# Kernel optimization log

Hardware: AMD Instinct MI355X
Metric: run time of the kernel (lower is better)

Reference implementation:

```python
import jax, jax.numpy as jnp
import numpy as np

B, T, I, H, O = 256, 512, 128, 512, 64
ALPHA = 0.2          # cfg.leak
BETA = 8.0           # cfg.softplus_beta
THRESH = 20.0        # cfg.softplus_threshold


def _phi(x):
    # F.softplus(x, beta, threshold): linear when beta*x > threshold
    z = BETA * x
    return jnp.where(z > THRESH, x, jax.nn.softplus(jnp.minimum(z, THRESH)) / BETA)


def setup_inputs() -> dict:
    key = jax.random.key(0)
    ks = jax.random.split(key, 6)
    x = jax.random.normal(ks[0], (B, T, I), dtype=jnp.float32)
    W_xh = jax.random.normal(ks[1], (H, I), dtype=jnp.float32) * (1.0 / np.sqrt(I))
    # E/I structure: column-wise sign (abs weights * sign), scaled to modest spectral radius
    sign = np.ones(H, dtype=np.float32)
    perm = np.random.default_rng(0).permutation(H)
    sign[perm[int(round(0.8 * H)):]] = -1.0
    W_hh = jnp.abs(jax.random.normal(ks[2], (H, H), dtype=jnp.float32)) * jnp.asarray(sign)[None, :]
    W_hh = W_hh * (1.2 / (jnp.linalg.norm(W_hh, ord=2) + 1e-6))
    b_h = jnp.zeros((H,), dtype=jnp.float32)
    W_out = jax.random.normal(ks[3], (O, H), dtype=jnp.float32) * (1.0 / np.sqrt(H))
    b_out = jnp.zeros((O,), dtype=jnp.float32)
    return {"x": x, "W_xh": W_xh, "W_hh": W_hh, "b_h": b_h, "W_out": W_out, "b_out": b_out}


def reference(x, W_xh, W_hh, b_h, W_out, b_out):
    # precompute input projection: [B,T,H]
    xw = jnp.einsum('bti,hi->bth', x, W_xh)

    def step(h, xw_t):  # h: [B,H], xw_t: [B,H]
        pre = xw_t + h @ W_hh.T + b_h
        h = (1.0 - ALPHA) * h + ALPHA * _phi(pre)
        y = h @ W_out.T + b_out  # readout='all'
        return h, y

    h0 = jnp.zeros((x.shape[0], W_hh.shape[0]), dtype=x.dtype)
    _, ys = jax.lax.scan(step, h0, jnp.swapaxes(xw, 0, 1))  # ys: [T,B,O]
    return jnp.swapaxes(ys, 0, 1)  # [B,T,O]
```

## Files before the change

### kernel.cpp

```cpp
#include <hip/hip_runtime.h>


#define BB 256
#define TT 512
#define II 128
#define HH 512
#define OO 64
#define RG 16
#define JC 64
#define NG 16
#define NC 8

typedef _Float16 f16;
typedef f16 f16x8 __attribute__((ext_vector_type(8)));
typedef float f32x4 __attribute__((ext_vector_type(4)));

__global__ __launch_bounds__(256, 1)
void eirnn_persist(const float* __restrict__ x,
                   const float* __restrict__ Wxh,
                   const float* __restrict__ Whh,
                   const float* __restrict__ bh,
                   const float* __restrict__ Wout,
                   const float* __restrict__ bout,
                   float* __restrict__ yout,
                   unsigned long long* __restrict__ hbuf)
{
    const int tid  = threadIdx.x;
    const int bid  = blockIdx.x;
    const int wave = tid >> 6;
    const int lane = tid & 63;
    const int quad = lane >> 4;
    const int l16  = lane & 15;
    const int r    = bid >> 3;
    const int c    = bid & 7;
    const int rowbase = r * RG;
    const int jbase   = c * JC;
    const int myrow   = wave * 16 + l16;

    __shared__ __align__(16) f16 hg[2][RG][HH + 8];
    __shared__ __align__(16) f16 xsh[2][RG][II + 8];

    f16x8 bf[16];
    f16x8 xbf[4];
    f16x8 bfo[2];
    {
        const float* wp = Whh + (size_t)(jbase + myrow) * HH + quad * 8;
        #pragma unroll
        for (int ks = 0; ks < 16; ++ks) {
            float4 u = *(const float4*)(wp + ks * 32);
            float4 v = *(const float4*)(wp + ks * 32 + 4);
            f16x8 tv;
            tv[0]=(f16)u.x; tv[1]=(f16)u.y; tv[2]=(f16)u.z; tv[3]=(f16)u.w;
            tv[4]=(f16)v.x; tv[5]=(f16)v.y; tv[6]=(f16)v.z; tv[7]=(f16)v.w;
            bf[ks] = tv;
        }
        const float* wq = Wxh + (size_t)(jbase + myrow) * II + quad * 8;
        #pragma unroll
        for (int ks = 0; ks < 4; ++ks) {
            float4 u = *(const float4*)(wq + ks * 32);
            float4 v = *(const float4*)(wq + ks * 32 + 4);
            f16x8 tv;
            tv[0]=(f16)u.x; tv[1]=(f16)u.y; tv[2]=(f16)u.z; tv[3]=(f16)u.w;
            tv[4]=(f16)v.x; tv[5]=(f16)v.y; tv[6]=(f16)v.z; tv[7]=(f16)v.w;
            xbf[ks] = tv;
        }
        const float* wo = Wout + (size_t)myrow * HH + c * 64 + quad * 8;
        #pragma unroll
        for (int ks = 0; ks < 2; ++ks) {
            float4 u = *(const float4*)(wo + ks * 32);
            float4 v = *(const float4*)(wo + ks * 32 + 4);
            f16x8 tv;
            tv[0]=(f16)u.x; tv[1]=(f16)u.y; tv[2]=(f16)u.z; tv[3]=(f16)u.w;
            tv[4]=(f16)v.x; tv[5]=(f16)v.y; tv[6]=(f16)v.z; tv[7]=(f16)v.w;
            bfo[ks] = tv;
        }
    }
    const float biash = bh[jbase + myrow];
    const float biaso = (c == 0) ? bout[myrow] : 0.0f;

    for (int p = tid; p < RG * (HH + 8); p += 256)
        ((unsigned int*)hg)[p] = 0u;

    float hreg[4] = {0.f, 0.f, 0.f, 0.f};

    const int j8     = tid;
    const int gshard = j8 >> 5;

    float4 xpf0, xpf1;
    {
        int p0 = tid, p1 = tid + 256;
        xpf0 = ((const float4*)(x + ((size_t)(rowbase + (p0 >> 5)) * TT + 0) * II))[p0 & 31];
        xpf1 = ((const float4*)(x + ((size_t)(rowbase + (p1 >> 5)) * TT + 0) * II))[p1 & 31];
    }

    __syncthreads();

    for (int t = 0; t <= TT; ++t) {
        const int pcur = t & 1;

        if (t < TT) {
            int p0 = tid, p1 = tid + 256;
            f16* d0 = &xsh[pcur][p0 >> 5][(p0 & 31) * 4];
            d0[0]=(f16)xpf0.x; d0[1]=(f16)xpf0.y; d0[2]=(f16)xpf0.z; d0[3]=(f16)xpf0.w;
            f16* d1 = &xsh[pcur][p1 >> 5][(p1 & 31) * 4];
            d1[0]=(f16)xpf1.x; d1[1]=(f16)xpf1.y; d1[2]=(f16)xpf1.z; d1[3]=(f16)xpf1.w;
        }
        if (t + 1 < TT) {
            int p0 = tid, p1 = tid + 256;
            xpf0 = ((const float4*)(x + ((size_t)(rowbase + (p0 >> 5)) * TT + (t + 1)) * II))[p0 & 31];
            xpf1 = ((const float4*)(x + ((size_t)(rowbase + (p1 >> 5)) * TT + (t + 1)) * II))[p1 & 31];
        }
        if (t >= 1 && gshard != c) {
            const unsigned long long* src = hbuf
                + (size_t)pcur * (BB * HH / 2)
                + (size_t)rowbase * (HH / 2) + j8;
            const unsigned int tg = (unsigned)t;
            unsigned long long v[16];
            #pragma unroll
            for (int i = 0; i < 16; ++i)
                v[i] = __hip_atomic_load(src + (size_t)i * (HH / 2),
                                         __ATOMIC_RELAXED, __HIP_MEMORY_SCOPE_AGENT);
            for (;;) {
                bool any = false;
                #pragma unroll
                for (int i = 0; i < 16; ++i)
                    any |= ((unsigned)(v[i] >> 32) != tg);
                if (!any) break;
                #pragma unroll
                for (int i = 0; i < 16; ++i)
                    if ((unsigned)(v[i] >> 32) != tg)
                        v[i] = __hip_atomic_load(src + (size_t)i * (HH / 2),
                                                 __ATOMIC_RELAXED, __HIP_MEMORY_SCOPE_AGENT);
            }
            #pragma unroll
            for (int i = 0; i < 16; ++i)
                *(unsigned int*)&hg[pcur][i][j8 * 2] = (unsigned int)v[i];
        }
        __syncthreads();

        if (t < TT) {
            f32x4 acc0 = {0.f,0.f,0.f,0.f}, acc1 = {0.f,0.f,0.f,0.f};
            #pragma unroll
            for (int ks = 0; ks < 16; ks += 2) {
                f16x8 a0 = *(const f16x8*)&hg[pcur][l16][ks * 32 + quad * 8];
                f16x8 a1 = *(const f16x8*)&hg[pcur][l16][(ks + 1) * 32 + quad * 8];
                acc0 = __builtin_amdgcn_mfma_f32_16x16x32_f16(a0, bf[ks], acc0, 0, 0, 0);
                acc1 = __builtin_amdgcn_mfma_f32_16x16x32_f16(a1, bf[ks + 1], acc1, 0, 0, 0);
            }
            #pragma unroll
            for (int ks = 0; ks < 4; ks += 2) {
                f16x8 a0 = *(const f16x8*)&xsh[pcur][l16][ks * 32 + quad * 8];
                f16x8 a1 = *(const f16x8*)&xsh[pcur][l16][(ks + 1) * 32 + quad * 8];
                acc0 = __builtin_amdgcn_mfma_f32_16x16x32_f16(a0, xbf[ks], acc0, 0, 0, 0);
                acc1 = __builtin_amdgcn_mfma_f32_16x16x32_f16(a1, xbf[ks + 1], acc1, 0, 0, 0);
            }
            unsigned long long* dst64 = hbuf + (size_t)((t + 1) & 1) * (BB * HH / 2);
            const unsigned long long tagw = ((unsigned long long)(unsigned)(t + 1)) << 32;
            unsigned int hb[4];
            #pragma unroll
            for (int reg = 0; reg < 4; ++reg) {
                float pre = acc0[reg] + acc1[reg] + biash;
                float z = 8.f * pre;
                float ph = (z > 20.f) ? pre : (__logf(1.f + __expf(z)) * 0.125f);
                float hn = 0.8f * hreg[reg] + 0.2f * ph;
                hreg[reg] = hn;
                hb[reg] = (unsigned int)__builtin_bit_cast(unsigned short, (f16)hn);
            }
            #pragma unroll
            for (int reg = 0; reg < 4; ++reg) {
                unsigned int ob = (unsigned int)__shfl_xor((int)hb[reg], 1, 64);
                if ((lane & 1) == 0) {
                    unsigned int pair = hb[reg] | (ob << 16);
                    size_t eidx = (size_t)(rowbase + quad * 4 + reg) * HH + jbase + myrow;
                    __hip_atomic_store(dst64 + (eidx >> 1), tagw | (unsigned long long)pair,
                                       __ATOMIC_RELAXED, __HIP_MEMORY_SCOPE_AGENT);
                    *(unsigned int*)&hg[(t + 1) & 1][quad * 4 + reg][jbase + myrow] = pair;
                }
            }
        }

        if (t >= 1) {
            f32x4 ya = {0.f,0.f,0.f,0.f};
            f16x8 a0 = *(const f16x8*)&hg[pcur][l16][c * 64 + quad * 8];
            f16x8 a1 = *(const f16x8*)&hg[pcur][l16][c * 64 + 32 + quad * 8];
            ya = __builtin_amdgcn_mfma_f32_16x16x32_f16(a0, bfo[0], ya, 0, 0, 0);
            ya = __builtin_amdgcn_mfma_f32_16x16x32_f16(a1, bfo[1], ya, 0, 0, 0);
            #pragma unroll
            for (int reg = 0; reg < 4; ++reg)
                atomicAdd(yout + ((size_t)(rowbase + quad * 4 + reg) * TT + (t - 1)) * OO + myrow,
                          ya[reg] + biaso);
        }
    }
}

extern "C" void kernel_launch(void* const* d_in, const int* in_sizes, int n_in,
                              void* d_out, int out_size, void* d_ws, size_t ws_size,
                              hipStream_t stream)
{
    const float* x    = (const float*)d_in[0];
    const float* Wxh  = (const float*)d_in[1];
    const float* Whh  = (const float*)d_in[2];
    const float* bh   = (const float*)d_in[3];
    const float* Wout = (const float*)d_in[4];
    const float* bout = (const float*)d_in[5];
    float* yout = (float*)d_out;

    unsigned long long* hbuf = (unsigned long long*)d_ws;
    const size_t hbuf_bytes = (size_t)2 * BB * (HH / 2) * sizeof(unsigned long long);

    if (ws_size < hbuf_bytes) return;

    hipMemsetAsync(hbuf, 0, hbuf_bytes, stream);
    hipMemsetAsync(yout, 0, (size_t)out_size * sizeof(float), stream);

    eirnn_persist<<<dim3(NG * NC), dim3(256), 0, stream>>>(
        x, Wxh, Whh, bh, Wout, bout, yout, hbuf);
}
```

Before: 1.396 ms.

## Split hidden dimension across two 1024-thread blocks per row group instead of eight

```diff
diff --git a/kernel.cpp b/kernel.cpp
--- a/kernel.cpp
+++ b/kernel.cpp
@@ -7,15 +7,15 @@
 #define HH 512
 #define OO 64
 #define RG 16
-#define JC 64
+#define JC 256
 #define NG 16
-#define NC 8
+#define NC 2
 
 typedef _Float16 f16;
 typedef f16 f16x8 __attribute__((ext_vector_type(8)));
 typedef float f32x4 __attribute__((ext_vector_type(4)));
 
-__global__ __launch_bounds__(256, 1)
+__global__ __launch_bounds__(1024, 1)
 void eirnn_persist(const float* __restrict__ x,
                    const float* __restrict__ Wxh,
                    const float* __restrict__ Whh,
@@ -31,8 +31,8 @@
     const int lane = tid & 63;
     const int quad = lane >> 4;
     const int l16  = lane & 15;
-    const int r    = bid >> 3;
-    const int c    = bid & 7;
+    const int r    = bid >> 1;
+    const int c    = bid & 1;
     const int rowbase = r * RG;
     const int jbase   = c * JC;
     const int myrow   = wave * 16 + l16;
@@ -43,6 +43,8 @@
     f16x8 bf[16];
     f16x8 xbf[4];
     f16x8 bfo[2];
+    const int koff = c * 256 + (wave >> 2) * 64;
+    const int ocol = (wave & 3) * 16 + l16;
     {
         const float* wp = Whh + (size_t)(jbase + myrow) * HH + quad * 8;
         #pragma unroll
@@ -64,7 +66,7 @@
             tv[4]=(f16)v.x; tv[5]=(f16)v.y; tv[6]=(f16)v.z; tv[7]=(f16)v.w;
             xbf[ks] = tv;
         }
-        const float* wo = Wout + (size_t)myrow * HH + c * 64 + quad * 8;
+        const float* wo = Wout + (size_t)ocol * HH + koff + quad * 8;
         #pragma unroll
         for (int ks = 0; ks < 2; ++ks) {
             float4 u = *(const float4*)(wo + ks * 32);
@@ -76,120 +78,122 @@
         }
     }
     const float biash = bh[jbase + myrow];
-    const float biaso = (c == 0) ? bout[myrow] : 0.0f;
-
-    for (int p = tid; p < RG * (HH + 8); p += 256)
-        ((unsigned int*)hg)[p] = 0u;
+    const float biaso = (c == 0 && (wave >> 2) == 0) ? bout[ocol] : 0.0f;
+
+    for (int p4 = tid; p4 < RG * (HH + 8) / 2; p4 += 1024)
+        ((unsigned int*)hg)[p4] = 0u;
+
+    float4 xpf;
+    if (tid < 512) {
+        float4 v = ((const float4*)(x + ((size_t)(rowbase + (tid >> 5)) * TT + 0) * II))[tid & 31];
+        f16* d = &xsh[0][tid >> 5][(tid & 31) * 4];
+        d[0]=(f16)v.x; d[1]=(f16)v.y; d[2]=(f16)v.z; d[3]=(f16)v.w;
+        xpf = ((const float4*)(x + ((size_t)(rowbase + (tid >> 5)) * TT + 1) * II))[tid & 31];
+    }
 
     float hreg[4] = {0.f, 0.f, 0.f, 0.f};
 
-    const int j8     = tid;
-    const int gshard = j8 >> 5;
-
-    float4 xpf0, xpf1;
-    {
-        int p0 = tid, p1 = tid + 256;
-        xpf0 = ((const float4*)(x + ((size_t)(rowbase + (p0 >> 5)) * TT + 0) * II))[p0 & 31];
-        xpf1 = ((const float4*)(x + ((size_t)(rowbase + (p1 >> 5)) * TT + 0) * II))[p1 & 31];
-    }
-
-    __syncthreads();
-
-    for (int t = 0; t <= TT; ++t) {
-        const int pcur = t & 1;
-
-        if (t < TT) {
-            int p0 = tid, p1 = tid + 256;
-            f16* d0 = &xsh[pcur][p0 >> 5][(p0 & 31) * 4];
-            d0[0]=(f16)xpf0.x; d0[1]=(f16)xpf0.y; d0[2]=(f16)xpf0.z; d0[3]=(f16)xpf0.w;
-            f16* d1 = &xsh[pcur][p1 >> 5][(p1 & 31) * 4];
-            d1[0]=(f16)xpf1.x; d1[1]=(f16)xpf1.y; d1[2]=(f16)xpf1.z; d1[3]=(f16)xpf1.w;
-        }
-        if (t + 1 < TT) {
-            int p0 = tid, p1 = tid + 256;
-            xpf0 = ((const float4*)(x + ((size_t)(rowbase + (p0 >> 5)) * TT + (t + 1)) * II))[p0 & 31];
-            xpf1 = ((const float4*)(x + ((size_t)(rowbase + (p1 >> 5)) * TT + (t + 1)) * II))[p1 & 31];
-        }
-        if (t >= 1 && gshard != c) {
-            const unsigned long long* src = hbuf
-                + (size_t)pcur * (BB * HH / 2)
-                + (size_t)rowbase * (HH / 2) + j8;
-            const unsigned int tg = (unsigned)t;
-            unsigned long long v[16];
-            #pragma unroll
-            for (int i = 0; i < 16; ++i)
-                v[i] = __hip_atomic_load(src + (size_t)i * (HH / 2),
-                                         __ATOMIC_RELAXED, __HIP_MEMORY_SCOPE_AGENT);
-            for (;;) {
-                bool any = false;
-                #pragma unroll
-                for (int i = 0; i < 16; ++i)
-                    any |= ((unsigned)(v[i] >> 32) != tg);
-                if (!any) break;
-                #pragma unroll
-                for (int i = 0; i < 16; ++i)
-                    if ((unsigned)(v[i] >> 32) != tg)
-                        v[i] = __hip_atomic_load(src + (size_t)i * (HH / 2),
-                                                 __ATOMIC_RELAXED, __HIP_MEMORY_SCOPE_AGENT);
+    const int prow = tid >> 7;
+    const int pj   = (1 - c) * 128 + (tid & 127);
+
+    for (int t = 0; t < TT; ++t) {
+        const int p  = t & 1;
+        const int pn = p ^ 1;
+        __syncthreads();
+
+        f32x4 acc0 = {0.f,0.f,0.f,0.f}, acc1 = {0.f,0.f,0.f,0.f};
+        #pragma unroll
+        for (int ks = 0; ks < 16; ks += 2) {
+            f16x8 a0 = *(const f16x8*)&hg[p][l16][ks * 32 + quad * 8];
+            f16x8 a1 = *(const f16x8*)&hg[p][l16][(ks + 1) * 32 + quad * 8];
+            acc0 = __builtin_amdgcn_mfma_f32_16x16x32_f16(a0, bf[ks], acc0, 0, 0, 0);
+            acc1 = __builtin_amdgcn_mfma_f32_16x16x32_f16(a1, bf[ks + 1], acc1, 0, 0, 0);
+        }
+        #pragma unroll
+        for (int ks = 0; ks < 4; ks += 2) {
+            f16x8 a0 = *(const f16x8*)&xsh[p][l16][ks * 32 + quad * 8];
+            f16x8 a1 = *(const f16x8*)&xsh[p][l16][(ks + 1) * 32 + quad * 8];
+            acc0 = __builtin_amdgcn_mfma_f32_16x16x32_f16(a0, xbf[ks], acc0, 0, 0, 0);
+            acc1 = __builtin_amdgcn_mfma_f32_16x16x32_f16(a1, xbf[ks + 1], acc1, 0, 0, 0);
+        }
+
+        unsigned long long* dst64 = hbuf + (size_t)pn * (BB * HH / 2);
+        const unsigned long long tagw = ((unsigned long long)(unsigned)(t + 1)) << 32;
+        unsigned int hb[4];
+        #pragma unroll
+        for (int reg = 0; reg < 4; ++reg) {
+            float pre = acc0[reg] + acc1[reg] + biash;
+            float z = 8.f * pre;
+            float ph = (z > 20.f) ? pre : (__logf(1.f + __expf(z)) * 0.125f);
+            float hn = 0.8f * hreg[reg] + 0.2f * ph;
+            hreg[reg] = hn;
+            hb[reg] = (unsigned int)__builtin_bit_cast(unsigned short, (f16)hn);
+        }
+        #pragma unroll
+        for (int reg = 0; reg < 4; ++reg) {
+            unsigned int ob = (unsigned int)__shfl_xor((int)hb[reg], 1, 64);
+            if ((lane & 1) == 0) {
+                unsigned int pair = hb[reg] | (ob << 16);
+                size_t eidx = (size_t)(rowbase + quad * 4 + reg) * HH + jbase + myrow;
+                __hip_atomic_store(dst64 + (eidx >> 1), tagw | (unsigned long long)pair,
+                                   __ATOMIC_RELAXED, __HIP_MEMORY_SCOPE_AGENT);
+                *(unsigned int*)&hg[pn][quad * 4 + reg][jbase + myrow] = pair;
             }
-            #pragma unroll
-            for (int i = 0; i < 16; ++i)
-                *(unsigned int*)&hg[pcur][i][j8 * 2] = (unsigned int)v[i];
-        }
-        __syncthreads();
-
-        if (t < TT) {
-            f32x4 acc0 = {0.f,0.f,0.f,0.f}, acc1 = {0.f,0.f,0.f,0.f};
-            #pragma unroll
-            for (int ks = 0; ks < 16; ks += 2) {
-                f16x8 a0 = *(const f16x8*)&hg[pcur][l16][ks * 32 + quad * 8];
-                f16x8 a1 = *(const f16x8*)&hg[pcur][l16][(ks + 1) * 32 + quad * 8];
-                acc0 = __builtin_amdgcn_mfma_f32_16x16x32_f16(a0, bf[ks], acc0, 0, 0, 0);
-                acc1 = __builtin_amdgcn_mfma_f32_16x16x32_f16(a1, bf[ks + 1], acc1, 0, 0, 0);
-            }
-            #pragma unroll
-            for (int ks = 0; ks < 4; ks += 2) {
-                f16x8 a0 = *(const f16x8*)&xsh[pcur][l16][ks * 32 + quad * 8];
-                f16x8 a1 = *(const f16x8*)&xsh[pcur][l16][(ks + 1) * 32 + quad * 8];
-                acc0 = __builtin_amdgcn_mfma_f32_16x16x32_f16(a0, xbf[ks], acc0, 0, 0, 0);
-                acc1 = __builtin_amdgcn_mfma_f32_16x16x32_f16(a1, xbf[ks + 1], acc1, 0, 0, 0);
-            }
-            unsigned long long* dst64 = hbuf + (size_t)((t + 1) & 1) * (BB * HH / 2);
-            const unsigned long long tagw = ((unsigned long long)(unsigned)(t + 1)) << 32;
-            unsigned int hb[4];
-            #pragma unroll
-            for (int reg = 0; reg < 4; ++reg) {
-                float pre = acc0[reg] + acc1[reg] + biash;
-                float z = 8.f * pre;
-                float ph = (z > 20.f) ? pre : (__logf(1.f + __expf(z)) * 0.125f);
-                float hn = 0.8f * hreg[reg] + 0.2f * ph;
-                hreg[reg] = hn;
-                hb[reg] = (unsigned int)__builtin_bit_cast(unsigned short, (f16)hn);
-            }
-            #pragma unroll
-            for (int reg = 0; reg < 4; ++reg) {
-                unsigned int ob = (unsigned int)__shfl_xor((int)hb[reg], 1, 64);
-                if ((lane & 1) == 0) {
-                    unsigned int pair = hb[reg] | (ob << 16);
-                    size_t eidx = (size_t)(rowbase + quad * 4 + reg) * HH + jbase + myrow;
-                    __hip_atomic_store(dst64 + (eidx >> 1), tagw | (unsigned long long)pair,
-                                       __ATOMIC_RELAXED, __HIP_MEMORY_SCOPE_AGENT);
-                    *(unsigned int*)&hg[(t + 1) & 1][quad * 4 + reg][jbase + myrow] = pair;
-                }
-            }
+        }
+
+        const unsigned long long* psrc = hbuf + (size_t)pn * (BB * HH / 2)
+                                       + (size_t)rowbase * (HH / 2) + pj;
+        unsigned long long pv0 = __hip_atomic_load(psrc + (size_t)prow * (HH / 2),
+                                                   __ATOMIC_RELAXED, __HIP_MEMORY_SCOPE_AGENT);
+        unsigned long long pv1 = __hip_atomic_load(psrc + (size_t)(prow + 8) * (HH / 2),
+                                                   __ATOMIC_RELAXED, __HIP_MEMORY_SCOPE_AGENT);
+        asm volatile("" ::: "memory");
+
+        if (t + 1 < TT && tid < 512) {
+            f16* d = &xsh[pn][tid >> 5][(tid & 31) * 4];
+            d[0]=(f16)xpf.x; d[1]=(f16)xpf.y; d[2]=(f16)xpf.z; d[3]=(f16)xpf.w;
+            if (t + 2 < TT)
+                xpf = ((const float4*)(x + ((size_t)(rowbase + (tid >> 5)) * TT + (t + 2)) * II))[tid & 31];
         }
 
         if (t >= 1) {
             f32x4 ya = {0.f,0.f,0.f,0.f};
-            f16x8 a0 = *(const f16x8*)&hg[pcur][l16][c * 64 + quad * 8];
-            f16x8 a1 = *(const f16x8*)&hg[pcur][l16][c * 64 + 32 + quad * 8];
+            f16x8 a0 = *(const f16x8*)&hg[p][l16][koff + quad * 8];
+            f16x8 a1 = *(const f16x8*)&hg[p][l16][koff + 32 + quad * 8];
             ya = __builtin_amdgcn_mfma_f32_16x16x32_f16(a0, bfo[0], ya, 0, 0, 0);
             ya = __builtin_amdgcn_mfma_f32_16x16x32_f16(a1, bfo[1], ya, 0, 0, 0);
             #pragma unroll
             for (int reg = 0; reg < 4; ++reg)
-                atomicAdd(yout + ((size_t)(rowbase + quad * 4 + reg) * TT + (t - 1)) * OO + myrow,
+                atomicAdd(yout + ((size_t)(rowbase + quad * 4 + reg) * TT + (t - 1)) * OO + ocol,
                           ya[reg] + biaso);
         }
+
+        {
+            const unsigned int tg = (unsigned)(t + 1);
+            while ((unsigned)(pv0 >> 32) != tg || (unsigned)(pv1 >> 32) != tg) {
+                if ((unsigned)(pv0 >> 32) != tg)
+                    pv0 = __hip_atomic_load(psrc + (size_t)prow * (HH / 2),
+                                            __ATOMIC_RELAXED, __HIP_MEMORY_SCOPE_AGENT);
+                if ((unsigned)(pv1 >> 32) != tg)
+                    pv1 = __hip_atomic_load(psrc + (size_t)(prow + 8) * (HH / 2),
+                                            __ATOMIC_RELAXED, __HIP_MEMORY_SCOPE_AGENT);
+            }
+            *(unsigned int*)&hg[pn][prow][pj * 2]     = (unsigned int)pv0;
+            *(unsigned int*)&hg[pn][prow + 8][pj * 2] = (unsigned int)pv1;
+        }
+    }
+
+    __syncthreads();
+    {
+        f32x4 ya = {0.f,0.f,0.f,0.f};
+        f16x8 a0 = *(const f16x8*)&hg[0][l16][koff + quad * 8];
+        f16x8 a1 = *(const f16x8*)&hg[0][l16][koff + 32 + quad * 8];
+        ya = __builtin_amdgcn_mfma_f32_16x16x32_f16(a0, bfo[0], ya, 0, 0, 0);
+        ya = __builtin_amdgcn_mfma_f32_16x16x32_f16(a1, bfo[1], ya, 0, 0, 0);
+        #pragma unroll
+        for (int reg = 0; reg < 4; ++reg)
+            atomicAdd(yout + ((size_t)(rowbase + quad * 4 + reg) * TT + (TT - 1)) * OO + ocol,
+                      ya[reg] + biaso);
     }
 }
 
@@ -213,6 +217,6 @@
     hipMemsetAsync(hbuf, 0, hbuf_bytes, stream);
     hipMemsetAsync(yout, 0, (size_t)out_size * sizeof(float), stream);
 
-    eirnn_persist<<<dim3(NG * NC), dim3(256), 0, stream>>>(
+    eirnn_persist<<<dim3(NG * NC), dim3(1024), 0, stream>>>(
         x, Wxh, Whh, bh, Wout, bout, yout, hbuf);
 }
```

New measurement: 3.829 ms. 2.74x slower.

## Remap blocks to XCD-local row groups and poll hidden state with sc0 loads

Applied to the files above, without the earlier changes.

```diff
diff --git a/kernel.cpp b/kernel.cpp
--- a/kernel.cpp
+++ b/kernel.cpp
@@ -10,6 +10,7 @@
 #define JC 64
 #define NG 16
 #define NC 8
+#define NB (NG * NC)
 
 typedef _Float16 f16;
 typedef f16 f16x8 __attribute__((ext_vector_type(8)));
@@ -31,8 +32,9 @@
     const int lane = tid & 63;
     const int quad = lane >> 4;
     const int l16  = lane & 15;
-    const int r    = bid >> 3;
-    const int c    = bid & 7;
+    const int mm   = bid >> 3;
+    const int c    = mm >> 1;
+    const int r    = (bid & 7) * 2 + (mm & 1);
     const int rowbase = r * RG;
     const int jbase   = c * JC;
     const int myrow   = wave * 16 + l16;
@@ -115,26 +117,72 @@
                 + (size_t)pcur * (BB * HH / 2)
                 + (size_t)rowbase * (HH / 2) + j8;
             const unsigned int tg = (unsigned)t;
-            unsigned long long v[16];
-            #pragma unroll
-            for (int i = 0; i < 16; ++i)
-                v[i] = __hip_atomic_load(src + (size_t)i * (HH / 2),
-                                         __ATOMIC_RELAXED, __HIP_MEMORY_SCOPE_AGENT);
-            for (;;) {
-                bool any = false;
-                #pragma unroll
-                for (int i = 0; i < 16; ++i)
-                    any |= ((unsigned)(v[i] >> 32) != tg);
-                if (!any) break;
-                #pragma unroll
-                for (int i = 0; i < 16; ++i)
-                    if ((unsigned)(v[i] >> 32) != tg)
-                        v[i] = __hip_atomic_load(src + (size_t)i * (HH / 2),
-                                                 __ATOMIC_RELAXED, __HIP_MEMORY_SCOPE_AGENT);
-            }
-            #pragma unroll
-            for (int i = 0; i < 16; ++i)
-                *(unsigned int*)&hg[pcur][i][j8 * 2] = (unsigned int)v[i];
+            unsigned long long v0, v1, v2, v3, v4, v5, v6, v7;
+            unsigned long long v8, v9, v10, v11, v12, v13, v14, v15;
+            asm volatile(
+                "global_load_dwordx2 %0, %8, off sc0\n\t"
+                "global_load_dwordx2 %1, %9, off sc0\n\t"
+                "global_load_dwordx2 %2, %10, off sc0\n\t"
+                "global_load_dwordx2 %3, %11, off sc0\n\t"
+                "global_load_dwordx2 %4, %12, off sc0\n\t"
+                "global_load_dwordx2 %5, %13, off sc0\n\t"
+                "global_load_dwordx2 %6, %14, off sc0\n\t"
+                "global_load_dwordx2 %7, %15, off sc0"
+                : "=&v"(v0), "=&v"(v1), "=&v"(v2), "=&v"(v3),
+                  "=&v"(v4), "=&v"(v5), "=&v"(v6), "=&v"(v7)
+                : "v"((unsigned long long)(src)),
+                  "v"((unsigned long long)(src + 1 * (HH / 2))),
+                  "v"((unsigned long long)(src + 2 * (HH / 2))),
+                  "v"((unsigned long long)(src + 3 * (HH / 2))),
+                  "v"((unsigned long long)(src + 4 * (HH / 2))),
+                  "v"((unsigned long long)(src + 5 * (HH / 2))),
+                  "v"((unsigned long long)(src + 6 * (HH / 2))),
+                  "v"((unsigned long long)(src + 7 * (HH / 2))));
+            asm volatile(
+                "global_load_dwordx2 %0, %16, off sc0\n\t"
+                "global_load_dwordx2 %1, %17, off sc0\n\t"
+                "global_load_dwordx2 %2, %18, off sc0\n\t"
+                "global_load_dwordx2 %3, %19, off sc0\n\t"
+                "global_load_dwordx2 %4, %20, off sc0\n\t"
+                "global_load_dwordx2 %5, %21, off sc0\n\t"
+                "global_load_dwordx2 %6, %22, off sc0\n\t"
+                "global_load_dwordx2 %7, %23, off sc0\n\t"
+                "s_waitcnt vmcnt(0)"
+                : "=&v"(v8), "=&v"(v9), "=&v"(v10), "=&v"(v11),
+                  "=&v"(v12), "=&v"(v13), "=&v"(v14), "=&v"(v15),
+                  "+v"(v0), "+v"(v1), "+v"(v2), "+v"(v3),
+                  "+v"(v4), "+v"(v5), "+v"(v6), "+v"(v7)
+                : "v"((unsigned long long)(src + 8 * (HH / 2))),
+                  "v"((unsigned long long)(src + 9 * (HH / 2))),
+                  "v"((unsigned long long)(src + 10 * (HH / 2))),
+                  "v"((unsigned long long)(src + 11 * (HH / 2))),
+                  "v"((unsigned long long)(src + 12 * (HH / 2))),
+                  "v"((unsigned long long)(src + 13 * (HH / 2))),
+                  "v"((unsigned long long)(src + 14 * (HH / 2))),
+                  "v"((unsigned long long)(src + 15 * (HH / 2))));
+            __builtin_amdgcn_sched_barrier(0);
+
+            unsigned long long vv[16] = {v0,v1,v2,v3,v4,v5,v6,v7,
+                                         v8,v9,v10,v11,v12,v13,v14,v15};
+            #pragma unroll
+            for (int i = 0; i < 16; ++i) {
+                unsigned long long w = vv[i];
+                const unsigned long long* pp = src + (size_t)i * (HH / 2);
+                int rr = 0;
+                while ((unsigned)(w >> 32) != tg) {
+                    ++rr;
+                    if ((rr & 3) == 3) {
+                        w = __hip_atomic_load(pp, __ATOMIC_RELAXED,
+                                              __HIP_MEMORY_SCOPE_AGENT);
+                    } else {
+                        asm volatile(
+                            "global_load_dwordx2 %0, %1, off sc0\n\t"
+                            "s_waitcnt vmcnt(0)"
+                            : "=&v"(w) : "v"((unsigned long long)pp));
+                    }
+                }
+                *(unsigned int*)&hg[pcur][i][j8 * 2] = (unsigned int)w;
+            }
         }
         __syncthreads();
 
@@ -213,6 +261,6 @@
     hipMemsetAsync(hbuf, 0, hbuf_bytes, stream);
     hipMemsetAsync(yout, 0, (size_t)out_size * sizeof(float), stream);
 
-    eirnn_persist<<<dim3(NG * NC), dim3(256), 0, stream>>>(
+    eirnn_persist<<<dim3(NB), dim3(256), 0, stream>>>(
         x, Wxh, Whh, bh, Wout, bout, yout, hbuf);
 }
```

Result: slower. 2.018 ms (+44.6%).
